# Kernel optimization log

Measured on AMD Instinct MI355X. Metric: run time of the kernel, lower is better.

## Reference

```python
import jax, jax.numpy as jnp
import numpy as np

T = 100          # sequence length (number of GRU steps)
H = 50           # carry/hidden dim
Z = 10           # latent dim
OUT = Z + Z * (Z + 1) // 2  # 65: mean + tril Cholesky entries
LN_EPS = 1e-6    # flax LayerNorm default epsilon


def setup_inputs() -> dict:
    key = jax.random.key(0)
    ks = jax.random.split(key, 8)
    # Orthogonal-ish recurrent kernels via QR for well-conditioned dynamics
    def ortho(k):
        a = jax.random.normal(k, (H, H), dtype=jnp.float32)
        q, _ = jnp.linalg.qr(a)
        return q
    return {
        "carry_init": jax.random.normal(ks[0], (H,), dtype=jnp.float32),
        "W_hr": ortho(ks[1]), "b_hr": jnp.zeros((H,), jnp.float32),
        "s_r": jnp.ones((H,), jnp.float32), "o_r": jnp.zeros((H,), jnp.float32),
        "W_hz": ortho(ks[2]), "b_hz": jnp.zeros((H,), jnp.float32),
        "s_z": jnp.ones((H,), jnp.float32), "o_z": jnp.zeros((H,), jnp.float32),
        "W_hn": ortho(ks[3]), "b_hn": jnp.zeros((H,), jnp.float32),
        "s_n": jnp.ones((H,), jnp.float32), "o_n": jnp.zeros((H,), jnp.float32),
        "W_dense": jax.random.normal(ks[4], (H, OUT), jnp.float32) * (1.0 / jnp.sqrt(H)),
        "b_dense": jnp.zeros((OUT,), jnp.float32),
    }


def _layernorm(x, scale, bias):
    mu = jnp.mean(x, axis=-1, keepdims=True)
    var = jnp.mean(jnp.square(x - mu), axis=-1, keepdims=True)
    return (x - mu) * jax.lax.rsqrt(var + LN_EPS) * scale + bias


def reference(carry_init, W_hr, b_hr, s_r, o_r, W_hz, b_hz, s_z, o_z,
              W_hn, b_hn, s_n, o_n, W_dense, b_dense):
    # Input to the GRU is zeros((T,1)) -> cell ignores it entirely (no input kernel).
    def step(h, _):
        r = jax.nn.sigmoid(_layernorm(h @ W_hr + b_hr, s_r, o_r))
        z = jax.nn.sigmoid(_layernorm(h @ W_hz + b_hz, s_z, o_z))
        n = jnp.tanh(r * _layernorm(h @ W_hn + b_hn, s_n, o_n))
        new_h = (1.0 - z) * n + z * h
        return new_h, new_h

    _, hs = jax.lax.scan(step, carry_init, None, length=T)  # (T, H)
    out = hs @ W_dense + b_dense                              # (T, OUT)

    tril = jnp.tril_indices(Z)
    eye = jnp.eye(Z, dtype=out.dtype)

    def nat(x):
        mu, flat = x[:Z], x[Z:]
        L = jnp.zeros((Z, Z), dtype=x.dtype).at[tril].set(flat)
        d = jax.nn.softplus(jnp.diagonal(L))  # positive diagonal -> PD Sigma
        L = L.at[jnp.diag_indices(Z)].set(d)
        Sigma = L @ L.T
        # psd_solve: J = Sigma^{-1} via Cholesky solve
        J = jax.scipy.linalg.cho_solve((L, True), eye)
        h_nat = J @ mu
        return Sigma, mu, J, h_nat

    Sigma, mu, J, h_nat = jax.vmap(nat)(out)
    return Sigma, mu, J, h_nat
```

## Files before the change

kernel.cpp:

```cpp
#include <hip/hip_runtime.h>
#include <hip/hip_bf16.h>
#include <math.h>

#define T_STEPS 100
#define H_DIM   50
#define Z_DIM   10
#define OUT_DIM 65

typedef float v2f __attribute__((ext_vector_type(2)));

__device__ __forceinline__ float bcast_lane(float v, int lane) {
    return __uint_as_float(__builtin_amdgcn_readlane(__float_as_uint(v), lane));
}
template<int CTRL>
__device__ __forceinline__ float dpp_mov(float x) {
    return __uint_as_float((unsigned)__builtin_amdgcn_update_dpp(
        0, (int)__float_as_uint(x), CTRL, 0xF, 0xF, true));
}
#define DPP_SHR1    0x111
#define DPP_SHR2    0x112
#define DPP_SHR4    0x114
#define DPP_SHR8    0x118
#define DPP_BCAST15 0x142
#define DPP_BCAST31 0x143

__device__ __forceinline__ float fast_rcp(float x) { return __builtin_amdgcn_rcpf(x); }
__device__ __forceinline__ float fast_rsq(float x) { return __builtin_amdgcn_rsqf(x); }
__device__ __forceinline__ float fast_sigmoid(float x) {
    return fast_rcp(1.0f + __expf(-x));
}
__device__ __forceinline__ float fast_tanh(float y) {
    return 1.0f - 2.0f * fast_rcp(__expf(2.0f * y) + 1.0f);
}

__global__ __launch_bounds__(64, 1)
void gru_recur_kernel(
    const float* __restrict__ carry_init,
    const float* __restrict__ W_hr, const float* __restrict__ b_hr,
    const float* __restrict__ s_r,  const float* __restrict__ o_r,
    const float* __restrict__ W_hz, const float* __restrict__ b_hz,
    const float* __restrict__ s_z,  const float* __restrict__ o_z,
    const float* __restrict__ W_hn, const float* __restrict__ b_hn,
    const float* __restrict__ s_n,  const float* __restrict__ o_n,
    float* __restrict__ ws_h)
{
    const int  j     = threadIdx.x;
    const bool valid = (j < H_DIM);
    const int  jc    = valid ? j : 0;

    v2f   wrz[H_DIM];
    float wn [H_DIM];
    #pragma unroll
    for (int i = 0; i < H_DIM; ++i) {
        const float r = valid ? W_hr[i * H_DIM + jc] : 0.0f;
        const float z = valid ? W_hz[i * H_DIM + jc] : 0.0f;
        const float n = valid ? W_hn[i * H_DIM + jc] : 0.0f;
        wrz[i] = (v2f){ r, z };
        wn [i] = n;
    }
    #pragma unroll
    for (int i = 0; i < H_DIM; ++i) {
        double d = __builtin_bit_cast(double, wrz[i]);
        float  f = wn[i];
        asm volatile("" : "+v"(d), "+v"(f));
        wrz[i] = __builtin_bit_cast(v2f, d);
        wn [i] = f;
    }

    const float bjr = valid ? b_hr[jc] : 0.0f;
    const float bjz = valid ? b_hz[jc] : 0.0f;
    const float bjn = valid ? b_hn[jc] : 0.0f;
    const float sr  = s_r[jc], og_r = o_r[jc];
    const float sz  = s_z[jc], og_z = o_z[jc];
    const float sn  = s_n[jc], og_n = o_n[jc];

    float h = valid ? carry_init[jc] : 0.0f;
    const float invH = 1.0f / (float)H_DIM;

    #pragma unroll 1
    for (int t = 0; t < T_STEPS; ++t) {
        v2f   arz0 = (v2f){ bjr, bjz }, arz1 = (v2f){ 0.0f, 0.0f };
        float an0 = bjn, an1 = 0.0f;
        #pragma unroll
        for (int i = 0; i < H_DIM; i += 2) {
            const float h0 = bcast_lane(h, i);
            const float h1 = bcast_lane(h, i + 1);
            arz0 = __builtin_elementwise_fma((v2f){ h0, h0 }, wrz[i],     arz0);
            an0  = fmaf(h0, wn[i],     an0);
            arz1 = __builtin_elementwise_fma((v2f){ h1, h1 }, wrz[i + 1], arz1);
            an1  = fmaf(h1, wn[i + 1], an1);
        }
        const v2f   arzv = arz0 + arz1;
        const float ar = arzv.x, az = arzv.y, an = an0 + an1;

        float mr = ar, qr = ar * ar;
        float mz = az, qz = az * az;
        float mn = an, qn = an * an;
        #define STAGE(C)                                      \
            mr += dpp_mov<C>(mr); qr += dpp_mov<C>(qr);       \
            mz += dpp_mov<C>(mz); qz += dpp_mov<C>(qz);       \
            mn += dpp_mov<C>(mn); qn += dpp_mov<C>(qn);
        STAGE(DPP_SHR1) STAGE(DPP_SHR2) STAGE(DPP_SHR4)
        STAGE(DPP_SHR8) STAGE(DPP_BCAST15) STAGE(DPP_BCAST31)
        #undef STAGE
        mr = bcast_lane(mr, 63); qr = bcast_lane(qr, 63);
        mz = bcast_lane(mz, 63); qz = bcast_lane(qz, 63);
        mn = bcast_lane(mn, 63); qn = bcast_lane(qn, 63);

        const float mu_r  = mr * invH;
        const float var_r = fmaxf(qr * invH - mu_r * mu_r, 0.0f);
        const float g_r   = (ar - mu_r) * fast_rsq(var_r + 1e-6f) * sr + og_r;
        const float r     = fast_sigmoid(g_r);

        const float mu_z  = mz * invH;
        const float var_z = fmaxf(qz * invH - mu_z * mu_z, 0.0f);
        const float g_z   = (az - mu_z) * fast_rsq(var_z + 1e-6f) * sz + og_z;
        const float z     = fast_sigmoid(g_z);

        const float mu_n  = mn * invH;
        const float var_n = fmaxf(qn * invH - mu_n * mu_n, 0.0f);
        const float g_n   = (an - mu_n) * fast_rsq(var_n + 1e-6f) * sn + og_n;
        const float n     = fast_tanh(r * g_n);

        h = n + z * (h - n);
        ws_h[t * 64 + j] = h;
    }
}

__global__ __launch_bounds__(128)
void dense_nat_kernel(
    const float* __restrict__ W_dense, const float* __restrict__ b_dense,
    const float* __restrict__ ws_h, float* __restrict__ out)
{
    const int t   = blockIdx.x;
    const int tid = threadIdx.x;

    __shared__ float hloc[H_DIM];
    __shared__ float dl  [OUT_DIM];
    __shared__ float Lp  [55];
    __shared__ float Li  [55];
    __shared__ float Jsh [100];

    if (tid < H_DIM) hloc[tid] = ws_h[t * 64 + tid];
    __syncthreads();

    if (tid < OUT_DIM) {
        float acc = b_dense[tid];
        #pragma unroll
        for (int i = 0; i < H_DIM; ++i)
            acc = fmaf(hloc[i], W_dense[i * OUT_DIM + tid], acc);
        dl[tid] = acc;
    }
    __syncthreads();

    if (tid < 55) {
        float v = dl[Z_DIM + tid];
        const bool isd = (tid==0)|(tid==2)|(tid==5)|(tid==9)|(tid==14)|
                         (tid==20)|(tid==27)|(tid==35)|(tid==44)|(tid==54);
        if (isd) v = (v > 20.0f) ? v : log1pf(__expf(v));
        Lp[tid] = v;
    }
    __syncthreads();

    float* outSigma = out;
    float* outMu    = out + 10000;
    float* outJ     = out + 11000;
    float* outHnat  = out + 21000;

    int a = 0;
    {
        #pragma unroll
        for (int x = 1; x < Z_DIM; ++x)
            if (tid >= x * (x + 1) / 2) a = x;
    }
    const int b = tid - a * (a + 1) / 2;

    if (tid < 55) {
        float s = 0.0f;
        for (int k = 0; k <= b; ++k)
            s = fmaf(Lp[a * (a + 1) / 2 + k], Lp[b * (b + 1) / 2 + k], s);
        outSigma[t * 100 + a * 10 + b] = s;
        outSigma[t * 100 + b * 10 + a] = s;
    }
    if (tid >= 64 && tid < 64 + Z_DIM) outMu[t * 10 + (tid - 64)] = dl[tid - 64];
    __syncthreads();

    if (tid == 0) {
        #pragma unroll
        for (int i = 0; i < Z_DIM; ++i) {
            const float d = 1.0f / Lp[i * (i + 1) / 2 + i];
            #pragma unroll
            for (int k = 0; k < i; ++k) {
                float s = 0.0f;
                for (int m = k; m < i; ++m)
                    s = fmaf(Lp[i * (i + 1) / 2 + m], Li[m * (m + 1) / 2 + k], s);
                Li[i * (i + 1) / 2 + k] = -s * d;
            }
            Li[i * (i + 1) / 2 + i] = d;
        }
    }
    __syncthreads();

    if (tid < 55) {
        float s = 0.0f;
        for (int m = a; m < Z_DIM; ++m)
            s = fmaf(Li[m * (m + 1) / 2 + a], Li[m * (m + 1) / 2 + b], s);
        outJ[t * 100 + a * 10 + b] = s;
        outJ[t * 100 + b * 10 + a] = s;
        Jsh[a * 10 + b] = s;
        Jsh[b * 10 + a] = s;
    }
    __syncthreads();

    if (tid < Z_DIM) {
        float s = 0.0f;
        #pragma unroll
        for (int k = 0; k < Z_DIM; ++k)
            s = fmaf(Jsh[tid * 10 + k], dl[k], s);
        outHnat[t * 10 + tid] = s;
    }
}

extern "C" void kernel_launch(void* const* d_in, const int* in_sizes, int n_in,
                              void* d_out, int out_size, void* d_ws, size_t ws_size,
                              hipStream_t stream) {
    const float* p[15];
    for (int i = 0; i < 15; ++i) p[i] = (const float*)d_in[i];
    float* ws_h = (float*)d_ws;

    gru_recur_kernel<<<dim3(1), dim3(64), 0, stream>>>(
        p[0],
        p[1], p[2], p[3], p[4],
        p[5], p[6], p[7], p[8],
        p[9], p[10], p[11], p[12],
        ws_h);

    dense_nat_kernel<<<dim3(T_STEPS), dim3(128), 0, stream>>>(
        p[13], p[14], ws_h, (float*)d_out);
}
```

Baseline: 140.6 us.

## Stage GRU recurrent weights in LDS rows instead of registers

Moves the three 50x50 recurrent weight columns per lane out of VGPRs into a padded shared-memory row per lane (stride 164 floats), read each step with float4 LDS loads. The packed v2f FMA path is dropped in favor of scalar FMAs with one accumulator per gate. It aims to cut register pressure, but it adds LDS load latency on the serial 100-step critical path and lengthens the dependent FMA chains.

```diff
diff --git a/kernel.cpp b/kernel.cpp
--- a/kernel.cpp
+++ b/kernel.cpp
@@ -7,7 +7,9 @@
 #define Z_DIM   10
 #define OUT_DIM 65
 
-typedef float v2f __attribute__((ext_vector_type(2)));
+#define ROW_STRIDE 164
+#define SEC_Z      52
+#define SEC_N      104
 
 __device__ __forceinline__ float bcast_lane(float v, int lane) {
     return __uint_as_float(__builtin_amdgcn_readlane(__float_as_uint(v), lane));
@@ -44,28 +46,23 @@
     const float* __restrict__ s_n,  const float* __restrict__ o_n,
     float* __restrict__ ws_h)
 {
+    __shared__ float wl[64 * ROW_STRIDE];
+
     const int  j     = threadIdx.x;
     const bool valid = (j < H_DIM);
     const int  jc    = valid ? j : 0;
 
-    v2f   wrz[H_DIM];
-    float wn [H_DIM];
-    #pragma unroll
+    float* row = &wl[j * ROW_STRIDE];
+
+    #pragma unroll 1
     for (int i = 0; i < H_DIM; ++i) {
-        const float r = valid ? W_hr[i * H_DIM + jc] : 0.0f;
-        const float z = valid ? W_hz[i * H_DIM + jc] : 0.0f;
-        const float n = valid ? W_hn[i * H_DIM + jc] : 0.0f;
-        wrz[i] = (v2f){ r, z };
-        wn [i] = n;
-    }
-    #pragma unroll
-    for (int i = 0; i < H_DIM; ++i) {
-        double d = __builtin_bit_cast(double, wrz[i]);
-        float  f = wn[i];
-        asm volatile("" : "+v"(d), "+v"(f));
-        wrz[i] = __builtin_bit_cast(v2f, d);
-        wn [i] = f;
-    }
+        row[i]           = valid ? W_hr[i * H_DIM + j] : 0.0f;
+        row[SEC_Z + i]   = valid ? W_hz[i * H_DIM + j] : 0.0f;
+        row[SEC_N + i]   = valid ? W_hn[i * H_DIM + j] : 0.0f;
+    }
+    row[50]          = 0.0f; row[51]          = 0.0f;
+    row[SEC_Z + 50]  = 0.0f; row[SEC_Z + 51]  = 0.0f;
+    row[SEC_N + 50]  = 0.0f; row[SEC_N + 51]  = 0.0f;
 
     const float bjr = valid ? b_hr[jc] : 0.0f;
     const float bjz = valid ? b_hz[jc] : 0.0f;
@@ -79,46 +76,51 @@
 
     #pragma unroll 1
     for (int t = 0; t < T_STEPS; ++t) {
-        v2f   arz0 = (v2f){ bjr, bjz }, arz1 = (v2f){ 0.0f, 0.0f };
-        float an0 = bjn, an1 = 0.0f;
-        #pragma unroll
-        for (int i = 0; i < H_DIM; i += 2) {
-            const float h0 = bcast_lane(h, i);
-            const float h1 = bcast_lane(h, i + 1);
-            arz0 = __builtin_elementwise_fma((v2f){ h0, h0 }, wrz[i],     arz0);
-            an0  = fmaf(h0, wn[i],     an0);
-            arz1 = __builtin_elementwise_fma((v2f){ h1, h1 }, wrz[i + 1], arz1);
-            an1  = fmaf(h1, wn[i + 1], an1);
+        const float* r_ = row;
+        asm volatile("" : "+v"(r_));
+
+        float ar = bjr, az = bjz, an = bjn;
+        #pragma unroll
+        for (int c = 0; c < 13; ++c) {
+            const float4 qr = *(const float4*)(r_ + 4 * c);
+            const float4 qz = *(const float4*)(r_ + SEC_Z + 4 * c);
+            const float4 qn = *(const float4*)(r_ + SEC_N + 4 * c);
+            const float h0 = bcast_lane(h, 4 * c + 0);
+            const float h1 = bcast_lane(h, 4 * c + 1);
+            const float h2 = bcast_lane(h, 4 * c + 2);
+            const float h3 = bcast_lane(h, 4 * c + 3);
+            ar = fmaf(h0, qr.x, ar); az = fmaf(h0, qz.x, az); an = fmaf(h0, qn.x, an);
+            ar = fmaf(h1, qr.y, ar); az = fmaf(h1, qz.y, az); an = fmaf(h1, qn.y, an);
+            ar = fmaf(h2, qr.z, ar); az = fmaf(h2, qz.z, az); an = fmaf(h2, qn.z, an);
+            ar = fmaf(h3, qr.w, ar); az = fmaf(h3, qz.w, az); an = fmaf(h3, qn.w, an);
         }
-        const v2f   arzv = arz0 + arz1;
-        const float ar = arzv.x, az = arzv.y, an = an0 + an1;
-
-        float mr = ar, qr = ar * ar;
-        float mz = az, qz = az * az;
-        float mn = an, qn = an * an;
-        #define STAGE(C)                                      \
-            mr += dpp_mov<C>(mr); qr += dpp_mov<C>(qr);       \
-            mz += dpp_mov<C>(mz); qz += dpp_mov<C>(qz);       \
-            mn += dpp_mov<C>(mn); qn += dpp_mov<C>(qn);
+
+        float mr = ar, qrs = ar * ar;
+        float mz = az, qzs = az * az;
+        float mn = an, qns = an * an;
+        #define STAGE(C)                                        \
+            mr += dpp_mov<C>(mr); qrs += dpp_mov<C>(qrs);       \
+            mz += dpp_mov<C>(mz); qzs += dpp_mov<C>(qzs);       \
+            mn += dpp_mov<C>(mn); qns += dpp_mov<C>(qns);
         STAGE(DPP_SHR1) STAGE(DPP_SHR2) STAGE(DPP_SHR4)
         STAGE(DPP_SHR8) STAGE(DPP_BCAST15) STAGE(DPP_BCAST31)
         #undef STAGE
-        mr = bcast_lane(mr, 63); qr = bcast_lane(qr, 63);
-        mz = bcast_lane(mz, 63); qz = bcast_lane(qz, 63);
-        mn = bcast_lane(mn, 63); qn = bcast_lane(qn, 63);
+        mr = bcast_lane(mr, 63); qrs = bcast_lane(qrs, 63);
+        mz = bcast_lane(mz, 63); qzs = bcast_lane(qzs, 63);
+        mn = bcast_lane(mn, 63); qns = bcast_lane(qns, 63);
 
         const float mu_r  = mr * invH;
-        const float var_r = fmaxf(qr * invH - mu_r * mu_r, 0.0f);
+        const float var_r = fmaxf(qrs * invH - mu_r * mu_r, 0.0f);
         const float g_r   = (ar - mu_r) * fast_rsq(var_r + 1e-6f) * sr + og_r;
         const float r     = fast_sigmoid(g_r);
 
         const float mu_z  = mz * invH;
-        const float var_z = fmaxf(qz * invH - mu_z * mu_z, 0.0f);
+        const float var_z = fmaxf(qzs * invH - mu_z * mu_z, 0.0f);
         const float g_z   = (az - mu_z) * fast_rsq(var_z + 1e-6f) * sz + og_z;
         const float z     = fast_sigmoid(g_z);
 
         const float mu_n  = mn * invH;
-        const float var_n = fmaxf(qn * invH - mu_n * mu_n, 0.0f);
+        const float var_n = fmaxf(qns * invH - mu_n * mu_n, 0.0f);
         const float g_n   = (an - mu_n) * fast_rsq(var_n + 1e-6f) * sn + og_n;
         const float n     = fast_tanh(r * g_n);
 
```

New measurement: 193.9 us. +37.9%, slower.

## Use packed fp16 dot2 for GRU recurrent matvec

Applied to the files above, without the earlier changes.

Stores the three recurrent weight matrices as packed half2 pairs and computes the per-step matvec with v_dot2 fp16 instructions, taking one readlane of a packed (h_i, h_{i+1}) pair per two rows. Each lane's neighbour value comes from a DPP row shift after every step. This halves the readlanes and the FMA count on the serial critical path, but rounds weights and hidden state to fp16 with round-toward-zero, so error can build up over the 100 recurrent steps. The DPP row-shift-left also does not cross 16-lane row boundaries, so lanes 15, 31 and 47 may pack a wrong neighbour, which matters only if those lanes are read. They are odd, and only even lanes are read.

```diff
diff --git a/kernel.cpp b/kernel.cpp
--- a/kernel.cpp
+++ b/kernel.cpp
@@ -6,23 +6,47 @@
 #define H_DIM   50
 #define Z_DIM   10
 #define OUT_DIM 65
-
-typedef float v2f __attribute__((ext_vector_type(2)));
+#define KP      25
+
+typedef _Float16 half2v __attribute__((ext_vector_type(2)));
 
 __device__ __forceinline__ float bcast_lane(float v, int lane) {
     return __uint_as_float(__builtin_amdgcn_readlane(__float_as_uint(v), lane));
+}
+__device__ __forceinline__ unsigned readlane_u(unsigned v, int lane) {
+    return (unsigned)__builtin_amdgcn_readlane((int)v, lane);
 }
 template<int CTRL>
 __device__ __forceinline__ float dpp_mov(float x) {
     return __uint_as_float((unsigned)__builtin_amdgcn_update_dpp(
         0, (int)__float_as_uint(x), CTRL, 0xF, 0xF, true));
 }
-#define DPP_SHR1    0x111
-#define DPP_SHR2    0x112
-#define DPP_SHR4    0x114
-#define DPP_SHR8    0x118
-#define DPP_BCAST15 0x142
-#define DPP_BCAST31 0x143
+#define DPP_ROW_SHL1 0x101
+#define DPP_SHR1     0x111
+#define DPP_SHR2     0x112
+#define DPP_SHR4     0x114
+#define DPP_SHR8     0x118
+#define DPP_BCAST15  0x142
+#define DPP_BCAST31  0x143
+
+__device__ __forceinline__ unsigned pack_h2(float lo, float hi) {
+#if __has_builtin(__builtin_amdgcn_cvt_pkrtz)
+    return __builtin_bit_cast(unsigned, __builtin_amdgcn_cvt_pkrtz(lo, hi));
+#else
+    half2v p; p.x = (_Float16)lo; p.y = (_Float16)hi;
+    return __builtin_bit_cast(unsigned, p);
+#endif
+}
+__device__ __forceinline__ float fdot2h(unsigned a, unsigned b, float c) {
+#if __has_builtin(__builtin_amdgcn_fdot2)
+    return __builtin_amdgcn_fdot2(__builtin_bit_cast(half2v, a),
+                                  __builtin_bit_cast(half2v, b), c, false);
+#else
+    const half2v x = __builtin_bit_cast(half2v, a);
+    const half2v y = __builtin_bit_cast(half2v, b);
+    return fmaf((float)x.x, (float)y.x, fmaf((float)x.y, (float)y.y, c));
+#endif
+}
 
 __device__ __forceinline__ float fast_rcp(float x) { return __builtin_amdgcn_rcpf(x); }
 __device__ __forceinline__ float fast_rsq(float x) { return __builtin_amdgcn_rsqf(x); }
@@ -48,24 +72,20 @@
     const bool valid = (j < H_DIM);
     const int  jc    = valid ? j : 0;
 
-    v2f   wrz[H_DIM];
-    float wn [H_DIM];
+    unsigned wr[KP], wz[KP], wn[KP];
     #pragma unroll
-    for (int i = 0; i < H_DIM; ++i) {
-        const float r = valid ? W_hr[i * H_DIM + jc] : 0.0f;
-        const float z = valid ? W_hz[i * H_DIM + jc] : 0.0f;
-        const float n = valid ? W_hn[i * H_DIM + jc] : 0.0f;
-        wrz[i] = (v2f){ r, z };
-        wn [i] = n;
+    for (int k = 0; k < KP; ++k) {
+        const int i0 = 2 * k, i1 = 2 * k + 1;
+        wr[k] = pack_h2(valid ? W_hr[i0 * H_DIM + j] : 0.0f,
+                        valid ? W_hr[i1 * H_DIM + j] : 0.0f);
+        wz[k] = pack_h2(valid ? W_hz[i0 * H_DIM + j] : 0.0f,
+                        valid ? W_hz[i1 * H_DIM + j] : 0.0f);
+        wn[k] = pack_h2(valid ? W_hn[i0 * H_DIM + j] : 0.0f,
+                        valid ? W_hn[i1 * H_DIM + j] : 0.0f);
     }
     #pragma unroll
-    for (int i = 0; i < H_DIM; ++i) {
-        double d = __builtin_bit_cast(double, wrz[i]);
-        float  f = wn[i];
-        asm volatile("" : "+v"(d), "+v"(f));
-        wrz[i] = __builtin_bit_cast(v2f, d);
-        wn [i] = f;
-    }
+    for (int k = 0; k < KP; ++k)
+        asm volatile("" : "+v"(wr[k]), "+v"(wz[k]), "+v"(wn[k]));
 
     const float bjr = valid ? b_hr[jc] : 0.0f;
     const float bjz = valid ? b_hz[jc] : 0.0f;
@@ -77,21 +97,30 @@
     float h = valid ? carry_init[jc] : 0.0f;
     const float invH = 1.0f / (float)H_DIM;
 
+    float    hsl = dpp_mov<DPP_ROW_SHL1>(h);
+    unsigned hpk = pack_h2(h, hsl);
+
     #pragma unroll 1
     for (int t = 0; t < T_STEPS; ++t) {
-        v2f   arz0 = (v2f){ bjr, bjz }, arz1 = (v2f){ 0.0f, 0.0f };
+        float ar0 = bjr, ar1 = 0.0f;
+        float az0 = bjz, az1 = 0.0f;
         float an0 = bjn, an1 = 0.0f;
         #pragma unroll
-        for (int i = 0; i < H_DIM; i += 2) {
-            const float h0 = bcast_lane(h, i);
-            const float h1 = bcast_lane(h, i + 1);
-            arz0 = __builtin_elementwise_fma((v2f){ h0, h0 }, wrz[i],     arz0);
-            an0  = fmaf(h0, wn[i],     an0);
-            arz1 = __builtin_elementwise_fma((v2f){ h1, h1 }, wrz[i + 1], arz1);
-            an1  = fmaf(h1, wn[i + 1], an1);
+        for (int k = 0; k < KP; k += 2) {
+            const unsigned s0 = readlane_u(hpk, 2 * k);
+            ar0 = fdot2h(s0, wr[k], ar0);
+            az0 = fdot2h(s0, wz[k], az0);
+            an0 = fdot2h(s0, wn[k], an0);
+            if (k + 1 < KP) {
+                const unsigned s1 = readlane_u(hpk, 2 * (k + 1));
+                ar1 = fdot2h(s1, wr[k + 1], ar1);
+                az1 = fdot2h(s1, wz[k + 1], az1);
+                an1 = fdot2h(s1, wn[k + 1], an1);
+            }
         }
-        const v2f   arzv = arz0 + arz1;
-        const float ar = arzv.x, az = arzv.y, an = an0 + an1;
+        const float ar = ar0 + ar1;
+        const float az = az0 + az1;
+        const float an = an0 + an1;
 
         float mr = ar, qr = ar * ar;
         float mz = az, qz = az * az;
@@ -124,6 +153,9 @@
 
         h = n + z * (h - n);
         ws_h[t * 64 + j] = h;
+
+        hsl = dpp_mov<DPP_ROW_SHL1>(h);
+        hpk = pack_h2(h, hsl);
     }
 }
 
```

Result: faster. 137.5 us (-2.2%).
